# Kernel tuning notes

Hardware: AMD Instinct MI355X
Metric: run time of the kernel (lower is better)

## Reference

```python
import jax, jax.numpy as jnp
import numpy as np

B, S = 2, 2048          # 2 sequences of length 2048 (prefill, equal-length varlen batch)
H, HKV, D = 32, 1, 64   # query heads, kv heads (MQA), head size
HID = H * D             # 2048
T = B * S
SCALE = D ** -0.5


def setup_inputs() -> dict:
    key = jax.random.key(0)
    k1, k2, k3 = jax.random.split(key, 3)
    hidden_states = jax.random.normal(k1, (T, HID), dtype=jnp.float32)
    # rotary tables: positions restart per sequence, NeoX half-rotation, base 10000
    inv_freq = 1.0 / (10000.0 ** (jnp.arange(0, D, 2, dtype=jnp.float32) / D))  # [D/2]
    pos = jnp.tile(jnp.arange(S, dtype=jnp.float32), B)                          # [T]
    freqs = pos[:, None] * inv_freq[None, :]                                     # [T, D/2]
    cos = jnp.cos(freqs)[:, None, :]                                             # [T,1,D/2]
    sin = jnp.sin(freqs)[:, None, :]
    w_qkv = jax.random.normal(k2, ((H + 2 * HKV) * D, HID), dtype=jnp.float32) * (HID ** -0.5)
    w_dense = jax.random.normal(k3, (HID, H * D), dtype=jnp.float32) * (HID ** -0.5)
    return {"hidden_states": hidden_states, "cos": cos, "sin": sin,
            "w_qkv": w_qkv, "w_dense": w_dense}


def _rope(x, cos, sin):
    # x: [T, nh, D]; cos/sin: [T, 1, D/2]; NeoX-style half rotation
    x1, x2 = x[..., : D // 2], x[..., D // 2:]
    return jnp.concatenate([x1 * cos - x2 * sin, x2 * cos + x1 * sin], axis=-1)


def reference(hidden_states, cos, sin, w_qkv, w_dense):
    qkv = hidden_states @ w_qkv.T                                # [T, (H+2*HKV)*D]
    q, kvf = jnp.split(qkv, [H * D], axis=1)
    q = q.reshape(T, H, D)
    kv = kvf.reshape(T, 2, HKV, D)
    q = _rope(q, cos, sin)
    k = _rope(kv[:, 0], cos, sin)                                # [T, HKV, D]
    v = kv[:, 1]                                                 # [T, HKV, D]
    # varlen prefill attention: reshape to [B,S,...]; MQA broadcast kv over H heads
    qb = q.reshape(B, S, H, D)
    kb = k.reshape(B, S, HKV, D)[:, :, 0, :]                     # [B,S,D]
    vb = v.reshape(B, S, HKV, D)[:, :, 0, :]
    scores = jnp.einsum("bshd,btd->bhst", qb, kb) * SCALE        # [B,H,S,S]
    causal = jnp.tril(jnp.ones((S, S), dtype=bool))
    scores = jnp.where(causal[None, None], scores, jnp.float32(-1e30))
    probs = jax.nn.softmax(scores, axis=-1)
    attn = jnp.einsum("bhst,btd->bshd", probs, vb)               # [B,S,H,D]
    return attn.reshape(T, H * D) @ w_dense.T                    # [T, HID]
```

## Files before the change

### kernel.cpp

```cpp
#include <hip/hip_runtime.h>

#define BB   2
#define SS   2048
#define TT   4096
#define HH   32
#define DD   64
#define HIDN 2048
#define NQKV 2176
#define QK_SCALE_LOG2 0.1803368801f

#define AS1 __attribute__((address_space(1)))
#define AS3 __attribute__((address_space(3)))

typedef __attribute__((ext_vector_type(8))) short short8;
typedef __attribute__((ext_vector_type(4))) float f32x4;
typedef __attribute__((ext_vector_type(16))) float f32x16;
typedef __attribute__((ext_vector_type(4))) unsigned short ushort4_t;
typedef __attribute__((ext_vector_type(4))) unsigned int uint4_t;

__device__ inline unsigned short f2bf(float f) {
  unsigned int u = __builtin_bit_cast(unsigned int, f);
  u += 0x7FFFu + ((u >> 16) & 1u);
  return (unsigned short)(u >> 16);
}
__device__ inline float bf2f(unsigned short s) {
  unsigned int u = ((unsigned int)s) << 16;
  return __builtin_bit_cast(float, u);
}
__device__ inline float exp2fast(float x) { return __builtin_amdgcn_exp2f(x); }

__global__ __launch_bounds__(256)
void cvt_all_kernel(const float* __restrict__ hs, const float* __restrict__ wqkv,
                    const float* __restrict__ wd, unsigned short* __restrict__ out) {
  int i = blockIdx.x * 256 + threadIdx.x;
  if (i >= 4259840) return;
  const float* src; int off;
  if (i < 2097152)      { src = hs;   off = i; }
  else if (i < 3211264) { src = wqkv; off = i - 2097152; }
  else                  { src = wd;   off = i - 3211264; }
  float4 v = ((const float4*)src)[off];
  ushort4_t u = { f2bf(v.x), f2bf(v.y), f2bf(v.z), f2bf(v.w) };
  *(ushort4_t*)(out + (long)i * 4) = u;
}

__global__ __launch_bounds__(256)
void gemm_qkv_split(const unsigned short* __restrict__ A, const unsigned short* __restrict__ Bw,
                    unsigned short* __restrict__ qout, float* __restrict__ kvp) {
  __shared__ unsigned char lAB[65536];
  const int K = HIDN;
  const int tid  = threadIdx.x;
  const int lane = tid & 63;
  const int wv   = tid >> 6;
  const int wr   = wv >> 1, wc = wv & 1;
  const int g    = lane >> 4, qq = lane & 15;

  long bm0, bn0; int kbeg, kend, isQ = 0, ks = 0;
  const int bid = blockIdx.x;
  if (bid < 512) {
    const int swz = (bid & 7) * 64 + (bid >> 3);
    isQ = 1;
    bm0 = (long)(swz >> 4) * 128;
    bn0 = (long)(swz & 15) * 128;
    kbeg = 0; kend = 2048;
  } else {
    const int r = bid - 512;
    bm0 = (long)(r >> 1) * 128;
    bn0 = 2048;
    ks  = r & 1;
    kbeg = ks * 1024; kend = kbeg + 1024;
  }

  const int srow  = tid >> 4;
  const int scolu = ((((tid & 15) << 4) ^ ((srow & 15) << 4)) >> 1);

  f32x4 zero = {0.f, 0.f, 0.f, 0.f};
  f32x4 acc[4][4];
#pragma unroll
  for (int m = 0; m < 4; ++m)
#pragma unroll
    for (int n = 0; n < 4; ++n) acc[m][n] = zero;

  const unsigned short* aSrc = A  + (bm0 + srow) * K + scolu;
  const unsigned short* bSrc = Bw + (bn0 + srow) * K + scolu;
  const int rswz = qq << 4;

  for (int k0 = kbeg; k0 < kend; k0 += 128) {
    __syncthreads();
#pragma unroll
    for (int gg = 0; gg < 8; ++gg) {
      __builtin_amdgcn_global_load_lds(
          (const AS1 unsigned int*)(aSrc + k0 + (long)16 * gg * K),
          (AS3 unsigned int*)(lAB + gg * 4096 + wv * 1024), 16, 0, 0);
      __builtin_amdgcn_global_load_lds(
          (const AS1 unsigned int*)(bSrc + k0 + (long)16 * gg * K),
          (AS3 unsigned int*)(lAB + 32768 + gg * 4096 + wv * 1024), 16, 0, 0);
    }
    __syncthreads();

#pragma unroll
    for (int kss = 0; kss < 4; ++kss) {
      short8 af[4], bf[4];
#pragma unroll
      for (int m = 0; m < 4; ++m)
        af[m] = *(const short8*)(lAB + (wr * 64 + m * 16 + qq) * 256
                                     + ((kss * 64 + g * 16) ^ rswz));
#pragma unroll
      for (int n = 0; n < 4; ++n)
        bf[n] = *(const short8*)(lAB + 32768 + (wc * 64 + n * 16 + qq) * 256
                                     + ((kss * 64 + g * 16) ^ rswz));
#pragma unroll
      for (int m = 0; m < 4; ++m)
#pragma unroll
        for (int n = 0; n < 4; ++n)
          acc[m][n] = __builtin_amdgcn_mfma_f32_16x16x32_bf16(af[m], bf[n], acc[m][n], 0, 0, 0);
    }
  }

  if (isQ) {
#pragma unroll
    for (int m = 0; m < 4; ++m)
#pragma unroll
      for (int r = 0; r < 4; ++r) {
        long row = bm0 + wr * 64 + m * 16 + g * 4 + r;
#pragma unroll
        for (int n = 0; n < 4; ++n)
          qout[row * 2048 + bn0 + wc * 64 + n * 16 + qq] = f2bf(acc[m][n][r]);
      }
  } else {
    float* dst = kvp + (long)ks * (4096 * 128);
#pragma unroll
    for (int m = 0; m < 4; ++m)
#pragma unroll
      for (int r = 0; r < 4; ++r) {
        long row = bm0 + wr * 64 + m * 16 + g * 4 + r;
#pragma unroll
        for (int n = 0; n < 4; ++n)
          dst[row * 128 + wc * 64 + n * 16 + qq] = acc[m][n][r];
      }
  }
}

__global__ __launch_bounds__(256)
void gemm_dense(const unsigned short* __restrict__ A, const unsigned short* __restrict__ Bw,
                float* __restrict__ Cp, int M, int N, int K) {
  __shared__ unsigned char lAB[65536];
  const int tid  = threadIdx.x;
  const int lane = tid & 63;
  const int wv   = tid >> 6;
  const int wr   = wv >> 1, wc = wv & 1;
  const int g    = lane >> 4, qq = lane & 15;
  const int gx   = gridDim.x;
  const int nwg  = gx * gridDim.y;
  const int lid  = blockIdx.y * gx + blockIdx.x;
  const int swz  = (lid & 7) * (nwg >> 3) + (lid >> 3);
  const long bm0 = (long)(swz / gx) * 128;
  const long bn0 = (long)(swz % gx) * 128;
  const int srow  = tid >> 4;
  const int scolu = ((((tid & 15) << 4) ^ ((srow & 15) << 4)) >> 1);

  f32x4 zero = {0.f, 0.f, 0.f, 0.f};
  f32x4 acc[4][4];
#pragma unroll
  for (int m = 0; m < 4; ++m)
#pragma unroll
    for (int n = 0; n < 4; ++n) acc[m][n] = zero;

  const unsigned short* aSrc = A  + (bm0 + srow) * K + scolu;
  const unsigned short* bSrc = Bw + (bn0 + srow) * K + scolu;
  const int rswz = qq << 4;

  for (int k0 = 0; k0 < K; k0 += 128) {
    __syncthreads();
#pragma unroll
    for (int gg = 0; gg < 8; ++gg) {
      __builtin_amdgcn_global_load_lds(
          (const AS1 unsigned int*)(aSrc + k0 + (long)16 * gg * K),
          (AS3 unsigned int*)(lAB + gg * 4096 + wv * 1024), 16, 0, 0);
      __builtin_amdgcn_global_load_lds(
          (const AS1 unsigned int*)(bSrc + k0 + (long)16 * gg * K),
          (AS3 unsigned int*)(lAB + 32768 + gg * 4096 + wv * 1024), 16, 0, 0);
    }
    __syncthreads();

#pragma unroll
    for (int kss = 0; kss < 4; ++kss) {
      short8 af[4], bf[4];
#pragma unroll
      for (int m = 0; m < 4; ++m)
        af[m] = *(const short8*)(lAB + (wr * 64 + m * 16 + qq) * 256
                                     + ((kss * 64 + g * 16) ^ rswz));
#pragma unroll
      for (int n = 0; n < 4; ++n)
        bf[n] = *(const short8*)(lAB + 32768 + (wc * 64 + n * 16 + qq) * 256
                                     + ((kss * 64 + g * 16) ^ rswz));
#pragma unroll
      for (int m = 0; m < 4; ++m)
#pragma unroll
        for (int n = 0; n < 4; ++n)
          acc[m][n] = __builtin_amdgcn_mfma_f32_16x16x32_bf16(af[m], bf[n], acc[m][n], 0, 0, 0);
    }
  }

#pragma unroll
  for (int m = 0; m < 4; ++m)
#pragma unroll
    for (int r = 0; r < 4; ++r) {
      long row = bm0 + wr * 64 + m * 16 + g * 4 + r;
#pragma unroll
      for (int n = 0; n < 4; ++n)
        Cp[row * N + bn0 + wc * 64 + n * 16 + qq] = acc[m][n][r];
    }
}

__global__ __launch_bounds__(256)
void kv_rope_kernel(const float* __restrict__ kvp, const float* __restrict__ cosb,
                    const float* __restrict__ sinb, unsigned short* __restrict__ k_out,
                    unsigned short* __restrict__ v_out) {
  int idx = blockIdx.x * 256 + threadIdx.x;
  if (idx >= TT * 8) return;
  int t   = idx >> 3;
  int rem = idx & 7;
  int i0  = (rem & 3) * 8;
  const float* p0 = kvp + (long)t * 128;
  const float* p1 = kvp + 4096 * 128 + (long)t * 128;

  if ((rem >> 2) == 0) {
    float cv[8], sv[8];
    *(float4*)(cv)     = *(const float4*)(cosb + t * 32 + i0);
    *(float4*)(cv + 4) = *(const float4*)(cosb + t * 32 + i0 + 4);
    *(float4*)(sv)     = *(const float4*)(sinb + t * 32 + i0);
    *(float4*)(sv + 4) = *(const float4*)(sinb + t * 32 + i0 + 4);
    unsigned short* kr2 = k_out + (long)t * 64;
#pragma unroll
    for (int j = 0; j < 8; ++j) {
      float x1 = p0[i0 + j]      + p1[i0 + j];
      float x2 = p0[32 + i0 + j] + p1[32 + i0 + j];
      kr2[i0 + j]      = f2bf(x1 * cv[j] - x2 * sv[j]);
      kr2[32 + i0 + j] = f2bf(x2 * cv[j] + x1 * sv[j]);
    }
  } else {
    int bb = t >> 11, s = t & 2047;
    int tile = s >> 6, c = s & 63;
    long base = ((long)bb * 32 + tile) * 64;
#pragma unroll
    for (int j = 0; j < 8; ++j) {
      v_out[(base + i0 + j) * 64 + c]      = f2bf(p0[64 + i0 + j] + p1[64 + i0 + j]);
      v_out[(base + 32 + i0 + j) * 64 + c] = f2bf(p0[96 + i0 + j] + p1[96 + i0 + j]);
    }
  }
}

__global__ __launch_bounds__(256, 2)
void attn_kernel(const unsigned short* __restrict__ qs, const unsigned short* __restrict__ kr,
                 const unsigned short* __restrict__ vt, const float* __restrict__ cosb,
                 const float* __restrict__ sinb, unsigned short* __restrict__ ob) {
  __shared__ unsigned char lsm[65536];
  const int tid  = threadIdx.x;
  const int lane = tid & 63;
  const int wv   = tid >> 6;
  const int half = lane >> 5;
  const int qc   = lane & 31;
  const int h    = blockIdx.y * 4 + wv;
  const int b    = blockIdx.z;
  const int qtA  = blockIdx.x;
  const int qtB  = (SS / 32 - 1) - blockIdx.x;
  const int q0A  = qtA * 32, q0B = qtB * 32;
  const int nbB  = (q0B >> 8) + 1;

  const unsigned short* kb  = kr + (long)b * SS * 64;
  const unsigned short* vtb = vt + (long)b * (SS / 64) * 64 * 64;

  const int srow = tid >> 3;
  const int scol = ((((tid & 7) << 4) ^ ((srow & 7) << 4)) >> 1);

  const int rswz = (qc & 7) << 4;
  int roff[4];
#pragma unroll
  for (int i = 0; i < 4; ++i)
    roff[i] = qc * 128 + ((i * 32 + half * 16) ^ rswz);

  short8 qfA[4], qfB[4];
  {
    const long tA = (long)(b * SS + q0A + qc);
    const long tB = (long)(b * SS + q0B + qc);
    const unsigned short* qrA = qs + (tA * HH + h) * 64;
    const unsigned short* qrB = qs + (tB * HH + h) * 64;
    short8 rA[4], rB[4];
#pragma unroll
    for (int dstep = 0; dstep < 4; ++dstep) {
      rA[dstep] = *(const short8*)(qrA + dstep * 16 + half * 8);
      rB[dstep] = *(const short8*)(qrB + dstep * 16 + half * 8);
    }
    float cvA[16], svA[16], cvB[16], svB[16];
#pragma unroll
    for (int s = 0; s < 2; ++s) {
      const int io = s * 16 + half * 8;
      *(float4*)(cvA + s * 8)     = *(const float4*)(cosb + tA * 32 + io);
      *(float4*)(cvA + s * 8 + 4) = *(const float4*)(cosb + tA * 32 + io + 4);
      *(float4*)(svA + s * 8)     = *(const float4*)(sinb + tA * 32 + io);
      *(float4*)(svA + s * 8 + 4) = *(const float4*)(sinb + tA * 32 + io + 4);
      *(float4*)(cvB + s * 8)     = *(const float4*)(cosb + tB * 32 + io);
      *(float4*)(cvB + s * 8 + 4) = *(const float4*)(cosb + tB * 32 + io + 4);
      *(float4*)(svB + s * 8)     = *(const float4*)(sinb + tB * 32 + io);
      *(float4*)(svB + s * 8 + 4) = *(const float4*)(sinb + tB * 32 + io + 4);
    }
#pragma unroll
    for (int s = 0; s < 2; ++s)
#pragma unroll
      for (int j = 0; j < 8; ++j) {
        float c_ = cvA[s * 8 + j], s_ = svA[s * 8 + j];
        float x1 = bf2f((unsigned short)rA[s][j]);
        float x2 = bf2f((unsigned short)rA[s + 2][j]);
        qfA[s][j]     = (short)f2bf((x1 * c_ - x2 * s_) * QK_SCALE_LOG2);
        qfA[s + 2][j] = (short)f2bf((x2 * c_ + x1 * s_) * QK_SCALE_LOG2);
        c_ = cvB[s * 8 + j]; s_ = svB[s * 8 + j];
        x1 = bf2f((unsigned short)rB[s][j]);
        x2 = bf2f((unsigned short)rB[s + 2][j]);
        qfB[s][j]     = (short)f2bf((x1 * c_ - x2 * s_) * QK_SCALE_LOG2);
        qfB[s + 2][j] = (short)f2bf((x2 * c_ + x1 * s_) * QK_SCALE_LOG2);
      }
  }

  f32x16 oA0, oA1, oB0, oB1;
#pragma unroll
  for (int r = 0; r < 16; ++r) { oA0[r] = 0.f; oA1[r] = 0.f; oB0[r] = 0.f; oB1[r] = 0.f; }
  float mA = -1e30f, lA = 0.f, mB = -1e30f, lB = 0.f;

#define PHASE(qf, o0, o1, mst, lst, q0x, maskNeeded)                             \
  do {                                                                           \
    f32x16 st0, st1;                                                             \
    _Pragma("unroll")                                                            \
    for (int r = 0; r < 16; ++r) { st0[r] = 0.f; st1[r] = 0.f; }                 \
    __builtin_amdgcn_s_setprio(1);                                               \
    _Pragma("unroll")                                                            \
    for (int dstep = 0; dstep < 4; ++dstep) {                                    \
      short8 kfA_ = *(const short8*)(Kb + roff[dstep]);                          \
      short8 kfB_ = *(const short8*)(Kb + roff[dstep] + 4096);                   \
      st0 = __builtin_amdgcn_mfma_f32_32x32x16_bf16(kfA_, qf[dstep], st0, 0, 0, 0); \
      st1 = __builtin_amdgcn_mfma_f32_32x32x16_bf16(kfB_, qf[dstep], st1, 0, 0, 0); \
    }                                                                            \
    __builtin_amdgcn_s_setprio(0);                                               \
    if (maskNeeded) {                                                            \
      _Pragma("unroll")                                                          \
      for (int r = 0; r < 16; ++r) {                                             \
        int rkv = (r & 3) + 8 * (r >> 2) + 4 * half;                             \
        if (kvb + rkv      > (q0x) + qc) st0[r] = -1e30f;                        \
        if (kvb + 32 + rkv > (q0x) + qc) st1[r] = -1e30f;                        \
      }                                                                          \
    }                                                                            \
    float pmax = st0[0];                                                         \
    _Pragma("unroll")                                                            \
    for (int r = 1; r < 16; ++r) pmax = fmaxf(pmax, st0[r]);                     \
    _Pragma("unroll")                                                            \
    for (int r = 0; r < 16; ++r) pmax = fmaxf(pmax, st1[r]);                     \
    pmax = fmaxf(pmax, __shfl_xor(pmax, 32));                                    \
    if (!__all(pmax - mst <= 8.f)) {                                             \
      const float mnew = fmaxf(mst, pmax);                                       \
      const float scal = exp2fast(mst - mnew);                                   \
      lst *= scal;                                                               \
      _Pragma("unroll")                                                          \
      for (int r = 0; r < 16; ++r) { o0[r] *= scal; o1[r] *= scal; }             \
      mst = mnew;                                                                \
    }                                                                            \
    float psum = 0.f;                                                            \
    _Pragma("unroll")                                                            \
    for (int r = 0; r < 16; ++r) { st0[r] = exp2fast(st0[r] - mst); psum += st0[r]; } \
    _Pragma("unroll")                                                            \
    for (int r = 0; r < 16; ++r) { st1[r] = exp2fast(st1[r] - mst); psum += st1[r]; } \
    psum += __shfl_xor(psum, 32);                                                \
    lst += psum;                                                                 \
    short8 pb[4];                                                                \
    _Pragma("unroll")                                                            \
    for (int hseg = 0; hseg < 2; ++hseg) {                                       \
      const f32x16& pp = hseg ? st1 : st0;                                       \
      unsigned int a0, a1, a2, a3, a4, a5, a6, a7;                               \
      asm("v_cvt_pk_bf16_f32 %0, %1, %2" : "=v"(a0) : "v"(pp[0]),  "v"(pp[1]));  \
      asm("v_cvt_pk_bf16_f32 %0, %1, %2" : "=v"(a1) : "v"(pp[2]),  "v"(pp[3]));  \
      asm("v_cvt_pk_bf16_f32 %0, %1, %2" : "=v"(a2) : "v"(pp[4]),  "v"(pp[5]));  \
      asm("v_cvt_pk_bf16_f32 %0, %1, %2" : "=v"(a3) : "v"(pp[6]),  "v"(pp[7]));  \
      asm("v_cvt_pk_bf16_f32 %0, %1, %2" : "=v"(a4) : "v"(pp[8]),  "v"(pp[9]));  \
      asm("v_cvt_pk_bf16_f32 %0, %1, %2" : "=v"(a5) : "v"(pp[10]), "v"(pp[11])); \
      asm("v_cvt_pk_bf16_f32 %0, %1, %2" : "=v"(a6) : "v"(pp[12]), "v"(pp[13])); \
      asm("v_cvt_pk_bf16_f32 %0, %1, %2" : "=v"(a7) : "v"(pp[14]), "v"(pp[15])); \
      asm("v_permlane32_swap_b32 %0, %1" : "+v"(a0), "+v"(a2));                  \
      asm("v_permlane32_swap_b32 %0, %1" : "+v"(a1), "+v"(a3));                  \
      asm("v_permlane32_swap_b32 %0, %1" : "+v"(a4), "+v"(a6));                  \
      asm("v_permlane32_swap_b32 %0, %1" : "+v"(a5), "+v"(a7));                  \
      uint4_t w0 = { a0, a1, a2, a3 };                                           \
      uint4_t w1 = { a4, a5, a6, a7 };                                           \
      pb[hseg * 2]     = __builtin_bit_cast(short8, w0);                         \
      pb[hseg * 2 + 1] = __builtin_bit_cast(short8, w1);                         \
    }                                                                            \
    __builtin_amdgcn_s_setprio(1);                                               \
    _Pragma("unroll")                                                            \
    for (int kss = 0; kss < 4; ++kss) {                                          \
      short8 vfA_ = *(const short8*)(Vb + roff[kss]);                            \
      short8 vfB_ = *(const short8*)(Vb + roff[kss] + 4096);                     \
      o0 = __builtin_amdgcn_mfma_f32_32x32x16_bf16(vfA_, pb[kss], o0, 0, 0, 0);  \
      o1 = __builtin_amdgcn_mfma_f32_32x32x16_bf16(vfB_, pb[kss], o1, 0, 0, 0);  \
    }                                                                            \
    __builtin_amdgcn_s_setprio(0);                                               \
  } while (0)

  for (int ib = 0; ib < nbB; ++ib) {
    const int kv0 = ib * 256;
    __syncthreads();
    {
      const unsigned short* kS = kb + ((long)(kv0 + srow)) * 64 + scol;
#pragma unroll
      for (int gg = 0; gg < 8; ++gg)
        __builtin_amdgcn_global_load_lds((const AS1 unsigned int*)(kS + gg * 32 * 64),
            (AS3 unsigned int*)(lsm + gg * 4096 + wv * 1024), 16, 0, 0);
      const unsigned short* vS = vtb + (long)(4 * ib) * 4096 + srow * 64 + scol;
#pragma unroll
      for (int gg = 0; gg < 8; ++gg)
        __builtin_amdgcn_global_load_lds((const AS1 unsigned int*)(vS + gg * 32 * 64),
            (AS3 unsigned int*)(lsm + 32768 + gg * 4096 + wv * 1024), 16, 0, 0);
    }
    __syncthreads();

    for (int ph = 0; ph < 4; ++ph) {
      const int kvb = kv0 + ph * 64;
      if (kvb > q0B + 31) break;
      const unsigned char* Kb = lsm + ph * 8192;
      const unsigned char* Vb = lsm + 32768 + ph * 8192;
      PHASE(qfB, oB0, oB1, mB, lB, q0B, (kvb + 63 > q0B));
      if (kvb <= q0A + 31)
        PHASE(qfA, oA0, oA1, mA, lA, q0A, (kvb + 63 > q0A));
    }
  }
#undef PHASE

  {
    const float inv = 1.f / lA;
    unsigned short* orow = ob + ((long)(b * SS + q0A + qc) * HH + h) * 64;
#pragma unroll
    for (int r = 0; r < 16; ++r) {
      int d0 = (r & 3) + 8 * (r >> 2) + 4 * half;
      orow[d0]      = f2bf(oA0[r] * inv);
      orow[32 + d0] = f2bf(oA1[r] * inv);
    }
  }
  {
    const float inv = 1.f / lB;
    unsigned short* orow = ob + ((long)(b * SS + q0B + qc) * HH + h) * 64;
#pragma unroll
    for (int r = 0; r < 16; ++r) {
      int d0 = (r & 3) + 8 * (r >> 2) + 4 * half;
      orow[d0]      = f2bf(oB0[r] * inv);
      orow[32 + d0] = f2bf(oB1[r] * inv);
    }
  }
}

extern "C" void kernel_launch(void* const* d_in, const int* in_sizes, int n_in,
                              void* d_out, int out_size, void* d_ws, size_t ws_size,
                              hipStream_t stream) {
  const float* hs   = (const float*)d_in[0];
  const float* cosb = (const float*)d_in[1];
  const float* sinb = (const float*)d_in[2];
  const float* wqkv = (const float*)d_in[3];
  const float* wd   = (const float*)d_in[4];

  char* ws = (char*)d_ws;
  unsigned short* hs_bf   = (unsigned short*)(ws);
  unsigned short* wqkv_bf = (unsigned short*)(ws + 16777216);
  unsigned short* wd_bf   = (unsigned short*)(ws + 25690112);
  unsigned short* q_bf    = (unsigned short*)(ws + 34078720);
  float*          kvp     = (float*)(ws + 50855936);
  unsigned short* k_bf    = (unsigned short*)(ws + 55050240);
  unsigned short* vt_bf   = (unsigned short*)(ws + 55574528);

  cvt_all_kernel<<<16640, 256, 0, stream>>>(hs, wqkv, wd, hs_bf);

  gemm_qkv_split<<<576, 256, 0, stream>>>(hs_bf, wqkv_bf, q_bf, kvp);

  kv_rope_kernel<<<128, 256, 0, stream>>>(kvp, cosb, sinb, k_bf, vt_bf);

  attn_kernel<<<dim3(SS / 64, 8, BB), 256, 0, stream>>>(q_bf, k_bf, vt_bf,
                                                        cosb, sinb, hs_bf);

  gemm_dense<<<dim3(16, 32), 256, 0, stream>>>(hs_bf, wd_bf, (float*)d_out,
                                               TT, HIDN, HIDN);
}
```

Measured before the change: 169.2 us.

## Fuse fp32-to-bf16 conversion into GEMM tile loads, drop separate convert kernel

Removes the standalone conversion kernel and has both GEMMs read fp32 inputs and weights directly, packing them to bf16 with v_cvt_pk_bf16_f32 before storing into LDS. This avoids writing and re-reading about 17 MB of bf16 copies and saves one launch. In exchange each GEMM tile load now reads twice the bytes from global memory. It also goes through registers instead of the direct global-to-LDS path, and operands are re-converted for every tile that reuses them.

New measurement: 208.0 us. 1.23x slower.

```diff
diff --git a/kernel.cpp b/kernel.cpp
--- a/kernel.cpp
+++ b/kernel.cpp
@@ -29,22 +29,18 @@
 }
 __device__ inline float exp2fast(float x) { return __builtin_amdgcn_exp2f(x); }
 
+__device__ inline uint4_t pk8(float4 a, float4 b) {
+  unsigned int u0, u1, u2, u3;
+  asm("v_cvt_pk_bf16_f32 %0, %1, %2" : "=v"(u0) : "v"(a.x), "v"(a.y));
+  asm("v_cvt_pk_bf16_f32 %0, %1, %2" : "=v"(u1) : "v"(a.z), "v"(a.w));
+  asm("v_cvt_pk_bf16_f32 %0, %1, %2" : "=v"(u2) : "v"(b.x), "v"(b.y));
+  asm("v_cvt_pk_bf16_f32 %0, %1, %2" : "=v"(u3) : "v"(b.z), "v"(b.w));
+  uint4_t w = { u0, u1, u2, u3 };
+  return w;
+}
+
 __global__ __launch_bounds__(256)
-void cvt_all_kernel(const float* __restrict__ hs, const float* __restrict__ wqkv,
-                    const float* __restrict__ wd, unsigned short* __restrict__ out) {
-  int i = blockIdx.x * 256 + threadIdx.x;
-  if (i >= 4259840) return;
-  const float* src; int off;
-  if (i < 2097152)      { src = hs;   off = i; }
-  else if (i < 3211264) { src = wqkv; off = i - 2097152; }
-  else                  { src = wd;   off = i - 3211264; }
-  float4 v = ((const float4*)src)[off];
-  ushort4_t u = { f2bf(v.x), f2bf(v.y), f2bf(v.z), f2bf(v.w) };
-  *(ushort4_t*)(out + (long)i * 4) = u;
-}
-
-__global__ __launch_bounds__(256)
-void gemm_qkv_split(const unsigned short* __restrict__ A, const unsigned short* __restrict__ Bw,
+void gemm_qkv_split(const float* __restrict__ Af, const float* __restrict__ Bf,
                     unsigned short* __restrict__ qout, float* __restrict__ kvp) {
   __shared__ unsigned char lAB[65536];
   const int K = HIDN;
@@ -70,8 +66,8 @@
     kbeg = ks * 1024; kend = kbeg + 1024;
   }
 
-  const int srow  = tid >> 4;
-  const int scolu = ((((tid & 15) << 4) ^ ((srow & 15) << 4)) >> 1);
+  const int srow = tid >> 4;
+  const int ecol = 8 * ((tid & 15) ^ (srow & 15));
 
   f32x4 zero = {0.f, 0.f, 0.f, 0.f};
   f32x4 acc[4][4];
@@ -80,20 +76,22 @@
 #pragma unroll
     for (int n = 0; n < 4; ++n) acc[m][n] = zero;
 
-  const unsigned short* aSrc = A  + (bm0 + srow) * K + scolu;
-  const unsigned short* bSrc = Bw + (bn0 + srow) * K + scolu;
+  const float* aSrc = Af + (bm0 + srow) * (long)K + ecol;
+  const float* bSrc = Bf + (bn0 + srow) * (long)K + ecol;
   const int rswz = qq << 4;
 
   for (int k0 = kbeg; k0 < kend; k0 += 128) {
     __syncthreads();
 #pragma unroll
     for (int gg = 0; gg < 8; ++gg) {
-      __builtin_amdgcn_global_load_lds(
-          (const AS1 unsigned int*)(aSrc + k0 + (long)16 * gg * K),
-          (AS3 unsigned int*)(lAB + gg * 4096 + wv * 1024), 16, 0, 0);
-      __builtin_amdgcn_global_load_lds(
-          (const AS1 unsigned int*)(bSrc + k0 + (long)16 * gg * K),
-          (AS3 unsigned int*)(lAB + 32768 + gg * 4096 + wv * 1024), 16, 0, 0);
+      const float* ap = aSrc + k0 + (long)16 * gg * K;
+      const float* bp = bSrc + k0 + (long)16 * gg * K;
+      float4 a0 = *(const float4*)(ap);
+      float4 a1 = *(const float4*)(ap + 4);
+      float4 b0 = *(const float4*)(bp);
+      float4 b1 = *(const float4*)(bp + 4);
+      *(uint4_t*)(lAB + gg * 4096 + (tid << 4))         = pk8(a0, a1);
+      *(uint4_t*)(lAB + 32768 + gg * 4096 + (tid << 4)) = pk8(b0, b1);
     }
     __syncthreads();
 
@@ -141,7 +139,7 @@
 }
 
 __global__ __launch_bounds__(256)
-void gemm_dense(const unsigned short* __restrict__ A, const unsigned short* __restrict__ Bw,
+void gemm_dense(const unsigned short* __restrict__ A, const float* __restrict__ Bf,
                 float* __restrict__ Cp, int M, int N, int K) {
   __shared__ unsigned char lAB[65536];
   const int tid  = threadIdx.x;
@@ -156,7 +154,8 @@
   const long bm0 = (long)(swz / gx) * 128;
   const long bn0 = (long)(swz % gx) * 128;
   const int srow  = tid >> 4;
-  const int scolu = ((((tid & 15) << 4) ^ ((srow & 15) << 4)) >> 1);
+  const int ecol  = 8 * ((tid & 15) ^ (srow & 15));
+  const int scolu = ecol;
 
   f32x4 zero = {0.f, 0.f, 0.f, 0.f};
   f32x4 acc[4][4];
@@ -165,8 +164,8 @@
 #pragma unroll
     for (int n = 0; n < 4; ++n) acc[m][n] = zero;
 
-  const unsigned short* aSrc = A  + (bm0 + srow) * K + scolu;
-  const unsigned short* bSrc = Bw + (bn0 + srow) * K + scolu;
+  const unsigned short* aSrc = A + (bm0 + srow) * (long)K + scolu;
+  const float*          bSrc = Bf + (bn0 + srow) * (long)K + ecol;
   const int rswz = qq << 4;
 
   for (int k0 = 0; k0 < K; k0 += 128) {
@@ -176,9 +175,10 @@
       __builtin_amdgcn_global_load_lds(
           (const AS1 unsigned int*)(aSrc + k0 + (long)16 * gg * K),
           (AS3 unsigned int*)(lAB + gg * 4096 + wv * 1024), 16, 0, 0);
-      __builtin_amdgcn_global_load_lds(
-          (const AS1 unsigned int*)(bSrc + k0 + (long)16 * gg * K),
-          (AS3 unsigned int*)(lAB + 32768 + gg * 4096 + wv * 1024), 16, 0, 0);
+      const float* bp = bSrc + k0 + (long)16 * gg * K;
+      float4 b0 = *(const float4*)(bp);
+      float4 b1 = *(const float4*)(bp + 4);
+      *(uint4_t*)(lAB + 32768 + gg * 4096 + (tid << 4)) = pk8(b0, b1);
     }
     __syncthreads();
 
@@ -463,23 +463,19 @@
   const float* wd   = (const float*)d_in[4];
 
   char* ws = (char*)d_ws;
-  unsigned short* hs_bf   = (unsigned short*)(ws);
-  unsigned short* wqkv_bf = (unsigned short*)(ws + 16777216);
-  unsigned short* wd_bf   = (unsigned short*)(ws + 25690112);
-  unsigned short* q_bf    = (unsigned short*)(ws + 34078720);
-  float*          kvp     = (float*)(ws + 50855936);
-  unsigned short* k_bf    = (unsigned short*)(ws + 55050240);
-  unsigned short* vt_bf   = (unsigned short*)(ws + 55574528);
-
-  cvt_all_kernel<<<16640, 256, 0, stream>>>(hs, wqkv, wd, hs_bf);
-
-  gemm_qkv_split<<<576, 256, 0, stream>>>(hs_bf, wqkv_bf, q_bf, kvp);
+  unsigned short* q_bf  = (unsigned short*)(ws);
+  float*          kvp   = (float*)(ws + 16777216);
+  unsigned short* k_bf  = (unsigned short*)(ws + 20971520);
+  unsigned short* vt_bf = (unsigned short*)(ws + 21495808);
+  unsigned short* aout  = (unsigned short*)(ws + 22020096);
+
+  gemm_qkv_split<<<576, 256, 0, stream>>>(hs, wqkv, q_bf, kvp);
 
   kv_rope_kernel<<<128, 256, 0, stream>>>(kvp, cosb, sinb, k_bf, vt_bf);
 
   attn_kernel<<<dim3(SS / 64, 8, BB), 256, 0, stream>>>(q_bf, k_bf, vt_bf,
-                                                        cosb, sinb, hs_bf);
-
-  gemm_dense<<<dim3(16, 32), 256, 0, stream>>>(hs_bf, wd_bf, (float*)d_out,
+                                                        cosb, sinb, aout);
+
+  gemm_dense<<<dim3(16, 32), 256, 0, stream>>>(aout, wd, (float*)d_out,
                                                TT, HIDN, HIDN);
 }
```
